# Performance work log

Hardware: AMD Instinct MI355X
Metric: run time of the kernel (lower is better)

Reference implementation:

```python
import jax, jax.numpy as jnp
import numpy as np

N_NODES = 100000
N_EDGES = 1600000
N_GRAPHS = 512
HIDDEN = 128
N_CLASSES = 10


def setup_inputs() -> dict:
    key = jax.random.key(0)
    ks = jax.random.split(key, 12)
    edge_index = jax.random.randint(ks[0], (2, N_EDGES), 0, N_NODES, dtype=jnp.int32)
    batch = jnp.sort(jax.random.randint(ks[1], (N_NODES,), 0, N_GRAPHS, dtype=jnp.int32))
    def lin(k, fi, fo):
        return jax.random.normal(k, (fi, fo), jnp.float32) * (1.0 / np.sqrt(fi))
    return {
        "edge_index": edge_index,
        "batch": batch,
        "W0": lin(ks[2], 1, HIDDEN),
        "b0": jax.random.normal(ks[3], (HIDDEN,), jnp.float32) * 0.01,
        "W1": lin(ks[4], HIDDEN, HIDDEN),
        "b1": jax.random.normal(ks[5], (HIDDEN,), jnp.float32) * 0.01,
        "W2": lin(ks[6], HIDDEN, HIDDEN),
        "b2": jax.random.normal(ks[7], (HIDDEN,), jnp.float32) * 0.01,
        "Wp": lin(ks[8], HIDDEN, N_CLASSES),
        "bp": jax.random.normal(ks[9], (N_CLASSES,), jnp.float32) * 0.01,
    }


def _gcn_setup(edge_index, n_nodes):
    # add self-loops (PyG GCNConv default) and compute symmetric normalization
    loop = jnp.arange(n_nodes, dtype=edge_index.dtype)
    src = jnp.concatenate([edge_index[0], loop])  # [E+N]
    dst = jnp.concatenate([edge_index[1], loop])
    deg = jax.ops.segment_sum(jnp.ones_like(src, dtype=jnp.float32), dst,
                              num_segments=n_nodes)
    dinv = jnp.where(deg > 0, jax.lax.rsqrt(deg), 0.0)
    norm = dinv[src] * dinv[dst]  # [E+N]
    return src, dst, norm


def _gcn_conv(x, W, b, src, dst, norm, n_nodes):
    h = x @ W                                # [N, out]
    msg = h[src] * norm[:, None]             # gather + scale, [E+N, out]
    out = jax.ops.segment_sum(msg, dst, num_segments=n_nodes)
    return out + b


def reference(edge_index, batch, W0, b0, W1, b1, W2, b2, Wp, bp):
    n = batch.shape[0]
    src, dst, norm = _gcn_setup(edge_index, n)
    x = jnp.ones((n, 1), jnp.float32)  # forward() hardcodes ones as features
    for W, b in ((W0, b0), (W1, b1), (W2, b2)):
        x = jax.nn.relu(_gcn_conv(x, W, b, src, dst, norm, n))
        # dropout_p = 0.0 -> identity
    # scatter_mean pooling over graphs
    s = jax.ops.segment_sum(x, batch, num_segments=N_GRAPHS)
    cnt = jax.ops.segment_sum(jnp.ones((n,), jnp.float32), batch,
                              num_segments=N_GRAPHS)
    pooled = s / jnp.maximum(cnt, 1.0)[:, None]
    logits = pooled @ Wp + bp
    return jax.nn.log_softmax(logits, axis=1)
```

## Files before the change

### kernel.cpp

```cpp
#include <hip/hip_runtime.h>

#define HID 128
#define NG 512
#define NC 10
#define BSH 9
#define BSZ (1 << BSH)
#define TILE 4096
#define NOEDGE 0xFFFFFFFFu

typedef unsigned int u32;
typedef unsigned short u16;
typedef __attribute__((ext_vector_type(8))) short short8;
typedef __attribute__((ext_vector_type(4))) float f32x4;

static __device__ __forceinline__ int gtid() {
    return blockIdx.x * blockDim.x + threadIdx.x;
}

static __device__ __forceinline__ u16 f2bf(float f) {
    u32 u = __float_as_uint(f);
    u32 r = u + 0x7fffu + ((u >> 16) & 1u);
    return (u16)(r >> 16);
}
static __device__ __forceinline__ float bf2f(u32 s) {
    return __uint_as_float(s << 16);
}
static __device__ __forceinline__ void bf8_unpack(uint4 u, float* f) {
    f[0] = bf2f(u.x & 0xffffu); f[1] = bf2f(u.x >> 16);
    f[2] = bf2f(u.y & 0xffffu); f[3] = bf2f(u.y >> 16);
    f[4] = bf2f(u.z & 0xffffu); f[5] = bf2f(u.z >> 16);
    f[6] = bf2f(u.w & 0xffffu); f[7] = bf2f(u.w >> 16);
}

__global__ __launch_bounds__(256) void k_bhist(const int* __restrict__ dst,
                                               int* __restrict__ bcnt, int E, int NB) {
    __shared__ int cnt[256];
    int t = threadIdx.x;
    int e0 = blockIdx.x * TILE;
    for (int i = t; i < NB; i += 256) cnt[i] = 0;
    __syncthreads();
#pragma unroll
    for (int k = 0; k < 16; ++k) {
        int e = e0 + k * 256 + t;
        if (e < E) atomicAdd(&cnt[dst[e] >> BSH], 1);
    }
    __syncthreads();
    for (int i = t; i < NB; i += 256)
        if (cnt[i] > 0) atomicAdd(&bcnt[i], cnt[i]);
}

__global__ __launch_bounds__(256) void k_bscan(const int* __restrict__ bcnt,
                                               int* __restrict__ bbase,
                                               int* __restrict__ bcur, int NB, int E) {
    __shared__ int s[256];
    int t = threadIdx.x;
    int own = (t < NB) ? bcnt[t] : 0;
    s[t] = own;
    __syncthreads();
    for (int off = 1; off < 256; off <<= 1) {
        int v = (t >= off) ? s[t - off] : 0;
        __syncthreads();
        s[t] += v;
        __syncthreads();
    }
    if (t < NB) {
        int b = s[t] - own;
        bbase[t] = b;
        bcur[t] = b;
    }
    if (t == 0) bbase[NB] = E;
}

__global__ __launch_bounds__(256) void k_part1(const int* __restrict__ src,
                                               const int* __restrict__ dst,
                                               int* __restrict__ bcur,
                                               u32* __restrict__ tmp, int E, int NB) {
    __shared__ int cnt[256];
    __shared__ int base[256];
    int t = threadIdx.x;
    int e0 = blockIdx.x * TILE;
    for (int i = t; i < NB; i += 256) cnt[i] = 0;
    __syncthreads();
    u32 p_[16];
    int b_[16];
#pragma unroll
    for (int k = 0; k < 16; ++k) {
        int e = e0 + k * 256 + t;
        if (e < E) {
            int d = dst[e];
            p_[k] = ((u32)src[e] << BSH) | (u32)(d & (BSZ - 1));
            b_[k] = d >> BSH;
            atomicAdd(&cnt[b_[k]], 1);
        } else {
            b_[k] = -1;
        }
    }
    __syncthreads();
    for (int i = t; i < NB; i += 256) {
        if (cnt[i] > 0) base[i] = atomicAdd(&bcur[i], cnt[i]);
        cnt[i] = 0;
    }
    __syncthreads();
#pragma unroll
    for (int k = 0; k < 16; ++k) {
        if (b_[k] >= 0) {
            int pos = base[b_[k]] + atomicAdd(&cnt[b_[k]], 1);
            tmp[pos] = p_[k];
        }
    }
}

__global__ __launch_bounds__(512) void k_part2(const int* __restrict__ bbase,
                                               const u32* __restrict__ tmp,
                                               u32* __restrict__ packed,
                                               int* __restrict__ rowptr,
                                               float* __restrict__ dinv,
                                               int N, int NB) {
    __shared__ int cnt[BSZ];
    __shared__ int scn[BSZ];
    __shared__ int cur[BSZ];
    int b = blockIdx.x;
    int v0 = b << BSH;
    int nv = N - v0; if (nv > BSZ) nv = BSZ;
    int t = threadIdx.x;
    int e0 = bbase[b], e1 = bbase[b + 1];

    cnt[t] = 0;
    __syncthreads();
    for (int e = e0 + t; e < e1; e += 512)
        atomicAdd(&cnt[tmp[e] & (BSZ - 1)], 1);
    __syncthreads();
    int own = cnt[t];
    scn[t] = own;
    __syncthreads();
    for (int off = 1; off < BSZ; off <<= 1) {
        int v = (t >= off) ? scn[t - off] : 0;
        __syncthreads();
        scn[t] += v;
        __syncthreads();
    }
    int start = e0 + scn[t] - own;
    cur[t] = start;
    if (t < nv) {
        rowptr[v0 + t] = start;
        dinv[v0 + t] = rsqrtf(1.0f + (float)own);
    }
    if (b == NB - 1 && t == 0) rowptr[N] = e1;
    __syncthreads();
    for (int e = e0 + t; e < e1; e += 512) {
        u32 p = tmp[e];
        int pos = atomicAdd(&cur[p & (BSZ - 1)], 1);
        packed[pos] = p >> BSH;
    }
}

__global__ __launch_bounds__(256) void k_sl0(const int* __restrict__ rowptr,
                                             const u32* __restrict__ packed,
                                             const float* __restrict__ dinv,
                                             const float* __restrict__ W0,
                                             const float* __restrict__ b0,
                                             u16* __restrict__ x, int N) {
    int lane = threadIdx.x & 31;
    int v = (blockIdx.x * 256 + threadIdx.x) >> 5;
    if (v >= N) return;
    int r0 = rowptr[v], r1 = rowptr[v + 1];
    float s = 0.0f;
    for (int j = r0 + lane; j < r1; j += 32) s += dinv[packed[j]];
#pragma unroll
    for (int off = 16; off > 0; off >>= 1) s += __shfl_xor(s, off, 32);
    float di = dinv[v];
    s = di * (di + s);
    int d0 = lane * 4;
    float4 w = *(const float4*)&W0[d0];
    float4 b = *(const float4*)&b0[d0];
    float a0 = fmaxf(fmaf(s, w.x, b.x), 0.0f);
    float a1 = fmaxf(fmaf(s, w.y, b.y), 0.0f);
    float a2 = fmaxf(fmaf(s, w.z, b.z), 0.0f);
    float a3 = fmaxf(fmaf(s, w.w, b.w), 0.0f);
    uint2 o;
    o.x = (u32)f2bf(a0) | ((u32)f2bf(a1) << 16);
    o.y = (u32)f2bf(a2) | ((u32)f2bf(a3) << 16);
    *(uint2*)&x[(size_t)v * HID + d0] = o;
}

__global__ __launch_bounds__(256) void k_wt(const float* __restrict__ W,
                                            u16* __restrict__ Wt) {
    int t = gtid();
    if (t >= 2048) return;
    int n = t >> 4;
    int j = t & 15;
    int js = j ^ (n & 7);
    u32 w0 = (u32)f2bf(W[(j * 8 + 0) * HID + n]) | ((u32)f2bf(W[(j * 8 + 1) * HID + n]) << 16);
    u32 w1 = (u32)f2bf(W[(j * 8 + 2) * HID + n]) | ((u32)f2bf(W[(j * 8 + 3) * HID + n]) << 16);
    u32 w2 = (u32)f2bf(W[(j * 8 + 4) * HID + n]) | ((u32)f2bf(W[(j * 8 + 5) * HID + n]) << 16);
    u32 w3 = (u32)f2bf(W[(j * 8 + 6) * HID + n]) | ((u32)f2bf(W[(j * 8 + 7) * HID + n]) << 16);
    uint4 o = make_uint4(w0, w1, w2, w3);
    *(uint4*)&Wt[(size_t)n * HID + js * 8] = o;
}

__global__ __launch_bounds__(256) void k_gemm(const u16* __restrict__ x,
                                              const u16* __restrict__ Wt,
                                              const float* __restrict__ dinv,
                                              u16* __restrict__ q, int nrows) {
    __shared__ u16 Wl[HID * HID];
    int tid = threadIdx.x;
    for (int i = tid; i < 2048; i += 256)
        *(uint4*)&Wl[i * 8] = *(const uint4*)&Wt[i * 8];

    int w = tid >> 6;
    int l = tid & 63;
    int R0 = blockIdx.x * 64 + w * 16;
    int arow = R0 + (l & 15);
    int koff = (l >> 4) * 8;

    short8 a[4];
#pragma unroll
    for (int kb = 0; kb < 4; ++kb) {
        if (arow < nrows)
            a[kb] = *(const short8*)&x[(size_t)arow * HID + kb * 32 + koff];
        else
            a[kb] = (short8)0;
    }
    __syncthreads();

    int colbase = l & 15;
    int rowq = (l >> 4) * 4;
    float dv[4];
#pragma unroll
    for (int i = 0; i < 4; ++i) {
        int orow = R0 + rowq + i;
        dv[i] = (orow < nrows) ? dinv[orow] : 0.0f;
    }
#pragma unroll
    for (int cb = 0; cb < 8; ++cb) {
        f32x4 acc = {0.0f, 0.0f, 0.0f, 0.0f};
        int wrow = cb * 16 + (l & 15);
#pragma unroll
        for (int kb = 0; kb < 4; ++kb) {
            int j = (kb * 4 + (l >> 4)) ^ (wrow & 7);
            short8 b = *(const short8*)&Wl[wrow * HID + j * 8];
            acc = __builtin_amdgcn_mfma_f32_16x16x32_bf16(a[kb], b, acc, 0, 0, 0);
        }
#pragma unroll
        for (int i = 0; i < 4; ++i) {
            int orow = R0 + rowq + i;
            if (orow < nrows)
                q[(size_t)orow * HID + cb * 16 + colbase] = f2bf(acc[i] * dv[i]);
        }
    }
}

__global__ __launch_bounds__(256) void k_aggr(const u32* __restrict__ packed,
                                              const int* __restrict__ rowptr,
                                              const u16* __restrict__ q,
                                              const float* __restrict__ dinv,
                                              const float* __restrict__ b,
                                              u16* __restrict__ y, int N) {
    int lane = threadIdx.x & 31;
    int v = (blockIdx.x * 256 + threadIdx.x) >> 5;
    if (v >= N) return;
    int r0 = rowptr[v], r1 = rowptr[v + 1];
    int half = lane >> 4;
    int d8 = (lane & 15) * 8;

    float acc[8];
    if (half == 0) {
        uint4 qv = *(const uint4*)&q[(size_t)v * HID + d8];
        bf8_unpack(qv, acc);
    } else {
#pragma unroll
        for (int j = 0; j < 8; ++j) acc[j] = 0.0f;
    }

    for (int base = r0; base < r1; base += 32) {
        int idx = base + lane;
        u32 e = (idx < r1) ? packed[idx] : NOEDGE;
        int m = r1 - base; if (m > 32) m = 32;
        int iters = (m + 1) >> 1;
        int k = 0;
        for (; k + 2 <= iters; k += 2) {
            u32 s0 = __shfl(e, 2 * k + half, 32);
            u32 s1 = __shfl(e, 2 * k + 2 + half, 32);
            uint4 h0 = make_uint4(0, 0, 0, 0);
            uint4 h1 = make_uint4(0, 0, 0, 0);
            if (s0 != NOEDGE) h0 = *(const uint4*)&q[(size_t)s0 * HID + d8];
            if (s1 != NOEDGE) h1 = *(const uint4*)&q[(size_t)s1 * HID + d8];
            float f0[8], f1[8];
            bf8_unpack(h0, f0);
            bf8_unpack(h1, f1);
#pragma unroll
            for (int j = 0; j < 8; ++j) acc[j] += f0[j] + f1[j];
        }
        if (k < iters) {
            u32 s0 = __shfl(e, 2 * k + half, 32);
            if (s0 != NOEDGE) {
                uint4 h0 = *(const uint4*)&q[(size_t)s0 * HID + d8];
                float f0[8];
                bf8_unpack(h0, f0);
#pragma unroll
                for (int j = 0; j < 8; ++j) acc[j] += f0[j];
            }
        }
    }
#pragma unroll
    for (int j = 0; j < 8; ++j) acc[j] += __shfl_xor(acc[j], 16, 32);

    if (half == 0) {
        float dv = dinv[v];
        float4 b0 = *(const float4*)&b[d8];
        float4 b1 = *(const float4*)&b[d8 + 4];
        float o[8];
        o[0] = fmaxf(fmaf(acc[0], dv, b0.x), 0.0f);
        o[1] = fmaxf(fmaf(acc[1], dv, b0.y), 0.0f);
        o[2] = fmaxf(fmaf(acc[2], dv, b0.z), 0.0f);
        o[3] = fmaxf(fmaf(acc[3], dv, b0.w), 0.0f);
        o[4] = fmaxf(fmaf(acc[4], dv, b1.x), 0.0f);
        o[5] = fmaxf(fmaf(acc[5], dv, b1.y), 0.0f);
        o[6] = fmaxf(fmaf(acc[6], dv, b1.z), 0.0f);
        o[7] = fmaxf(fmaf(acc[7], dv, b1.w), 0.0f);
        uint4 u;
        u.x = (u32)f2bf(o[0]) | ((u32)f2bf(o[1]) << 16);
        u.y = (u32)f2bf(o[2]) | ((u32)f2bf(o[3]) << 16);
        u.z = (u32)f2bf(o[4]) | ((u32)f2bf(o[5]) << 16);
        u.w = (u32)f2bf(o[6]) | ((u32)f2bf(o[7]) << 16);
        *(uint4*)&y[(size_t)v * HID + d8] = u;
    }
}

__global__ __launch_bounds__(256) void k_pool(const u16* __restrict__ x,
                                              const int* __restrict__ batch,
                                              float* __restrict__ pooled,
                                              float* __restrict__ cntg, int N) {
    const int K = 32;
    int grp = threadIdx.x >> 4;
    int lane16 = threadIdx.x & 15;
    int d8 = lane16 * 8;
    int chunk = blockIdx.x * 16 + grp;
    int v0 = chunk * K;
    if (v0 >= N) return;
    int vend = v0 + K; if (vend > N) vend = N;
    int g = batch[v0];
    float acc[8] = {0, 0, 0, 0, 0, 0, 0, 0};
    float c = 0.0f;
    for (int v = v0; v < vend; ++v) {
        int gv = batch[v];
        if (gv != g) {
#pragma unroll
            for (int j = 0; j < 8; ++j) atomicAdd(&pooled[g * HID + d8 + j], acc[j]);
            if (lane16 == 0) atomicAdd(&cntg[g], c);
#pragma unroll
            for (int j = 0; j < 8; ++j) acc[j] = 0.0f;
            c = 0.0f; g = gv;
        }
        uint4 u = *(const uint4*)&x[(size_t)v * HID + d8];
        float f[8];
        bf8_unpack(u, f);
#pragma unroll
        for (int j = 0; j < 8; ++j) acc[j] += f[j];
        c += 1.0f;
    }
#pragma unroll
    for (int j = 0; j < 8; ++j) atomicAdd(&pooled[g * HID + d8 + j], acc[j]);
    if (lane16 == 0) atomicAdd(&cntg[g], c);
}

__global__ void k_head(const float* __restrict__ pooled, const float* __restrict__ cnt,
                       const float* __restrict__ Wp, const float* __restrict__ bp,
                       float* __restrict__ out) {
    int g = gtid();
    if (g >= NG) return;
    float inv = 1.0f / fmaxf(cnt[g], 1.0f);
    float l[NC];
#pragma unroll
    for (int c = 0; c < NC; ++c) l[c] = bp[c];
    for (int d = 0; d < HID; ++d) {
        float pv = pooled[g * HID + d] * inv;
#pragma unroll
        for (int c = 0; c < NC; ++c) l[c] = fmaf(pv, Wp[d * NC + c], l[c]);
    }
    float m = l[0];
#pragma unroll
    for (int c = 1; c < NC; ++c) m = fmaxf(m, l[c]);
    float s = 0.0f;
#pragma unroll
    for (int c = 0; c < NC; ++c) s += expf(l[c] - m);
    float ls = logf(s) + m;
#pragma unroll
    for (int c = 0; c < NC; ++c) out[g * NC + c] = l[c] - ls;
}

extern "C" void kernel_launch(void* const* d_in, const int* in_sizes, int n_in,
                              void* d_out, int out_size, void* d_ws, size_t ws_size,
                              hipStream_t stream) {
    const int* ei    = (const int*)d_in[0];
    int E            = in_sizes[0] / 2;
    const int* src   = ei;
    const int* dstp  = ei + E;
    const int* batch = (const int*)d_in[1];
    int N            = in_sizes[1];
    const float* W0  = (const float*)d_in[2];
    const float* b0  = (const float*)d_in[3];
    const float* W1  = (const float*)d_in[4];
    const float* b1  = (const float*)d_in[5];
    const float* W2  = (const float*)d_in[6];
    const float* b2  = (const float*)d_in[7];
    const float* Wp  = (const float*)d_in[8];
    const float* bp  = (const float*)d_in[9];
    float* out       = (float*)d_out;

    u16*  xA     = (u16*)d_ws;
    u16*  xB     = xA + (size_t)N * HID;
    u32*  packed = (u32*)(xB + (size_t)N * HID);
    u32*  tmp    = packed + E;
    u16*  Wt1    = (u16*)(tmp + E);
    u16*  Wt2    = Wt1 + HID * HID;
    int*  rowptr = (int*)(Wt2 + HID * HID);
    int*  bcnt   = rowptr + N + 1;
    int*  bbase  = bcnt + 256;
    int*  bcur   = bbase + 257;
    float* dinv  = (float*)(bcur + 256);
    float* pooled= dinv + N;
    float* cntg  = pooled + NG * HID;

    auto cdiv = [](int a, int b) { return (a + b - 1) / b; };
    int NB = cdiv(N, BSZ);

    hipMemsetAsync(bcnt, 0, 256 * sizeof(int), stream);
    hipMemsetAsync(pooled, 0, (NG * HID + NG) * sizeof(float), stream);

    k_bhist<<<cdiv(E, TILE), 256, 0, stream>>>(dstp, bcnt, E, NB);
    k_bscan<<<1, 256, 0, stream>>>(bcnt, bbase, bcur, NB, E);
    k_part1<<<cdiv(E, TILE), 256, 0, stream>>>(src, dstp, bcur, tmp, E, NB);
    k_part2<<<NB, 512, 0, stream>>>(bbase, tmp, packed, rowptr, dinv, N, NB);

    k_wt<<<8, 256, 0, stream>>>(W1, Wt1);
    k_wt<<<8, 256, 0, stream>>>(W2, Wt2);

    k_sl0<<<cdiv(N, 8), 256, 0, stream>>>(rowptr, packed, dinv, W0, b0, xA, N);

    k_gemm<<<cdiv(N, 64), 256, 0, stream>>>(xA, Wt1, dinv, xB, N);
    k_aggr<<<cdiv(N, 8), 256, 0, stream>>>(packed, rowptr, xB, dinv, b1, xA, N);

    k_gemm<<<cdiv(N, 64), 256, 0, stream>>>(xA, Wt2, dinv, xB, N);
    k_aggr<<<cdiv(N, 8), 256, 0, stream>>>(packed, rowptr, xB, dinv, b2, xA, N);

    k_pool<<<cdiv(cdiv(N, 32), 16), 256, 0, stream>>>(xA, batch, pooled, cntg, N);
    k_head<<<2, 256, 0, stream>>>(pooled, cntg, Wp, bp, out);
}
```

Before: 292.6 us.

## Precompute piecewise-linear layer-1 tables to skip first GEMM; widen aggregation to 64 lanes

New measurement: 326.0 us. 1.11x slower.

```diff
diff --git a/kernel.cpp b/kernel.cpp
--- a/kernel.cpp
+++ b/kernel.cpp
@@ -154,12 +154,70 @@
     }
 }
 
-__global__ __launch_bounds__(256) void k_sl0(const int* __restrict__ rowptr,
+__global__ __launch_bounds__(128) void k_sort(const float* __restrict__ W0,
+                                              const float* __restrict__ b0,
+                                              float* __restrict__ ts,
+                                              int* __restrict__ sidx) {
+    __shared__ float t[HID];
+    __shared__ int ix[HID];
+    int i = threadIdx.x;
+    float w = W0[i];
+    t[i] = (w != 0.0f) ? (-b0[i] / w) : 3.0e38f;
+    ix[i] = i;
+    __syncthreads();
+    for (int ph = 0; ph < HID; ++ph) {
+        int j = 2 * i + (ph & 1);
+        if (j + 1 < HID) {
+            if (t[j] > t[j + 1]) {
+                float tv = t[j]; t[j] = t[j + 1]; t[j + 1] = tv;
+                int iv = ix[j]; ix[j] = ix[j + 1]; ix[j + 1] = iv;
+            }
+        }
+        __syncthreads();
+    }
+    ts[i] = t[i];
+    sidx[i] = ix[i];
+}
+
+__global__ __launch_bounds__(128) void k_tab(const float* __restrict__ W0,
+                                             const float* __restrict__ b0,
+                                             const float* __restrict__ W1,
+                                             const int* __restrict__ sidx,
+                                             float* __restrict__ A,
+                                             float* __restrict__ Bt) {
+    __shared__ float w0s[HID], b0s[HID];
+    __shared__ int ds[HID];
+    int r = blockIdx.x;
+    int j = threadIdx.x;
+    ds[j] = sidx[j];
+    w0s[j] = W0[ds[j]];
+    b0s[j] = b0[ds[j]];
+    __syncthreads();
+    float a = 0.0f, b = 0.0f;
+    for (int p = 0; p < HID; ++p) {
+        int d = ds[p];
+        float w0 = w0s[p];
+        bool act = (w0 != 0.0f) ? ((w0 > 0.0f) ? (p < r) : (p >= r)) : (b0s[p] > 0.0f);
+        if (act) {
+            float w1 = W1[d * HID + j];
+            a = fmaf(w0, w1, a);
+            b = fmaf(b0s[p], w1, b);
+        }
+    }
+    A[r * HID + j] = a;
+    Bt[r * HID + j] = b;
+}
+
+__global__ __launch_bounds__(256) void k_l01(const int* __restrict__ rowptr,
                                              const u32* __restrict__ packed,
                                              const float* __restrict__ dinv,
-                                             const float* __restrict__ W0,
-                                             const float* __restrict__ b0,
-                                             u16* __restrict__ x, int N) {
+                                             const float* __restrict__ ts,
+                                             const float* __restrict__ A,
+                                             const float* __restrict__ Bt,
+                                             u16* __restrict__ q, int N) {
+    __shared__ float tls[HID];
+    if (threadIdx.x < HID) tls[threadIdx.x] = ts[threadIdx.x];
+    __syncthreads();
     int lane = threadIdx.x & 31;
     int v = (blockIdx.x * 256 + threadIdx.x) >> 5;
     if (v >= N) return;
@@ -170,17 +228,23 @@
     for (int off = 16; off > 0; off >>= 1) s += __shfl_xor(s, off, 32);
     float di = dinv[v];
     s = di * (di + s);
+    int lo = 0, hi = HID;
+    while (lo < hi) {
+        int mid = (lo + hi) >> 1;
+        if (tls[mid] < s) lo = mid + 1; else hi = mid;
+    }
+    int r = lo;
     int d0 = lane * 4;
-    float4 w = *(const float4*)&W0[d0];
-    float4 b = *(const float4*)&b0[d0];
-    float a0 = fmaxf(fmaf(s, w.x, b.x), 0.0f);
-    float a1 = fmaxf(fmaf(s, w.y, b.y), 0.0f);
-    float a2 = fmaxf(fmaf(s, w.z, b.z), 0.0f);
-    float a3 = fmaxf(fmaf(s, w.w, b.w), 0.0f);
+    float4 av = *(const float4*)&A[r * HID + d0];
+    float4 bv = *(const float4*)&Bt[r * HID + d0];
+    float q0 = di * fmaf(av.x, s, bv.x);
+    float q1 = di * fmaf(av.y, s, bv.y);
+    float q2 = di * fmaf(av.z, s, bv.z);
+    float q3 = di * fmaf(av.w, s, bv.w);
     uint2 o;
-    o.x = (u32)f2bf(a0) | ((u32)f2bf(a1) << 16);
-    o.y = (u32)f2bf(a2) | ((u32)f2bf(a3) << 16);
-    *(uint2*)&x[(size_t)v * HID + d0] = o;
+    o.x = (u32)f2bf(q0) | ((u32)f2bf(q1) << 16);
+    o.y = (u32)f2bf(q2) | ((u32)f2bf(q3) << 16);
+    *(uint2*)&q[(size_t)v * HID + d0] = o;
 }
 
 __global__ __launch_bounds__(256) void k_wt(const float* __restrict__ W,
@@ -256,15 +320,15 @@
                                               const float* __restrict__ dinv,
                                               const float* __restrict__ b,
                                               u16* __restrict__ y, int N) {
-    int lane = threadIdx.x & 31;
-    int v = (blockIdx.x * 256 + threadIdx.x) >> 5;
+    int lane = threadIdx.x & 63;
+    int v = (blockIdx.x * 256 + threadIdx.x) >> 6;
     if (v >= N) return;
     int r0 = rowptr[v], r1 = rowptr[v + 1];
-    int half = lane >> 4;
+    int q4 = lane >> 4;
     int d8 = (lane & 15) * 8;
 
     float acc[8];
-    if (half == 0) {
+    if (q4 == 0) {
         uint4 qv = *(const uint4*)&q[(size_t)v * HID + d8];
         bf8_unpack(qv, acc);
     } else {
@@ -272,15 +336,15 @@
         for (int j = 0; j < 8; ++j) acc[j] = 0.0f;
     }
 
-    for (int base = r0; base < r1; base += 32) {
+    for (int base = r0; base < r1; base += 64) {
         int idx = base + lane;
         u32 e = (idx < r1) ? packed[idx] : NOEDGE;
-        int m = r1 - base; if (m > 32) m = 32;
-        int iters = (m + 1) >> 1;
+        int m = r1 - base; if (m > 64) m = 64;
+        int iters = (m + 3) >> 2;
         int k = 0;
         for (; k + 2 <= iters; k += 2) {
-            u32 s0 = __shfl(e, 2 * k + half, 32);
-            u32 s1 = __shfl(e, 2 * k + 2 + half, 32);
+            u32 s0 = __shfl(e, 4 * k + q4, 64);
+            u32 s1 = __shfl(e, 4 * k + 4 + q4, 64);
             uint4 h0 = make_uint4(0, 0, 0, 0);
             uint4 h1 = make_uint4(0, 0, 0, 0);
             if (s0 != NOEDGE) h0 = *(const uint4*)&q[(size_t)s0 * HID + d8];
@@ -292,7 +356,7 @@
             for (int j = 0; j < 8; ++j) acc[j] += f0[j] + f1[j];
         }
         if (k < iters) {
-            u32 s0 = __shfl(e, 2 * k + half, 32);
+            u32 s0 = __shfl(e, 4 * k + q4, 64);
             if (s0 != NOEDGE) {
                 uint4 h0 = *(const uint4*)&q[(size_t)s0 * HID + d8];
                 float f0[8];
@@ -303,9 +367,12 @@
         }
     }
 #pragma unroll
-    for (int j = 0; j < 8; ++j) acc[j] += __shfl_xor(acc[j], 16, 32);
-
-    if (half == 0) {
+    for (int j = 0; j < 8; ++j) {
+        acc[j] += __shfl_xor(acc[j], 16, 64);
+        acc[j] += __shfl_xor(acc[j], 32, 64);
+    }
+
+    if (q4 == 0) {
         float dv = dinv[v];
         float4 b0 = *(const float4*)&b[d8];
         float4 b1 = *(const float4*)&b[d8 + 4];
@@ -412,9 +479,12 @@
     u16*  xB     = xA + (size_t)N * HID;
     u32*  packed = (u32*)(xB + (size_t)N * HID);
     u32*  tmp    = packed + E;
-    u16*  Wt1    = (u16*)(tmp + E);
-    u16*  Wt2    = Wt1 + HID * HID;
-    int*  rowptr = (int*)(Wt2 + HID * HID);
+    u16*  Wt2    = (u16*)(tmp + E);
+    float* A     = (float*)(Wt2 + HID * HID);
+    float* Bt    = A + 129 * HID;
+    float* ts    = Bt + 129 * HID;
+    int*  sidx   = (int*)(ts + HID);
+    int*  rowptr = sidx + HID;
     int*  bcnt   = rowptr + N + 1;
     int*  bbase  = bcnt + 256;
     int*  bcur   = bbase + 257;
@@ -433,16 +503,16 @@
     k_part1<<<cdiv(E, TILE), 256, 0, stream>>>(src, dstp, bcur, tmp, E, NB);
     k_part2<<<NB, 512, 0, stream>>>(bbase, tmp, packed, rowptr, dinv, N, NB);
 
-    k_wt<<<8, 256, 0, stream>>>(W1, Wt1);
+    k_sort<<<1, 128, 0, stream>>>(W0, b0, ts, sidx);
+    k_tab<<<129, 128, 0, stream>>>(W0, b0, W1, sidx, A, Bt);
     k_wt<<<8, 256, 0, stream>>>(W2, Wt2);
 
-    k_sl0<<<cdiv(N, 8), 256, 0, stream>>>(rowptr, packed, dinv, W0, b0, xA, N);
-
-    k_gemm<<<cdiv(N, 64), 256, 0, stream>>>(xA, Wt1, dinv, xB, N);
-    k_aggr<<<cdiv(N, 8), 256, 0, stream>>>(packed, rowptr, xB, dinv, b1, xA, N);
+    k_l01<<<cdiv(N, 8), 256, 0, stream>>>(rowptr, packed, dinv, ts, A, Bt, xB, N);
+
+    k_aggr<<<cdiv(N, 4), 256, 0, stream>>>(packed, rowptr, xB, dinv, b1, xA, N);
 
     k_gemm<<<cdiv(N, 64), 256, 0, stream>>>(xA, Wt2, dinv, xB, N);
-    k_aggr<<<cdiv(N, 8), 256, 0, stream>>>(packed, rowptr, xB, dinv, b2, xA, N);
+    k_aggr<<<cdiv(N, 4), 256, 0, stream>>>(packed, rowptr, xB, dinv, b2, xA, N);
 
     k_pool<<<cdiv(cdiv(N, 32), 16), 256, 0, stream>>>(xA, batch, pooled, cntg, N);
     k_head<<<2, 256, 0, stream>>>(pooled, cntg, Wp, bp, out);
```
